# Performance work log

Measured on AMD Instinct MI355X. Metric: run time of the kernel, lower is better.

Reference implementation:

```python
import jax, jax.numpy as jnp
import numpy as np

VOCAB = 50257
EMBED = 128
B, S = 64, 4096


def setup_inputs() -> dict:
    key = jax.random.key(0)
    k1, k2, k3 = jax.random.split(key, 3)
    x = jax.random.randint(k1, (B, S), 0, VOCAB)
    # Linear(n_symboles, output_size) weight has shape [output_size, n_symboles]
    W = jax.random.normal(k2, (EMBED, VOCAB), dtype=jnp.float32) * 0.02
    b = jax.random.normal(k3, (EMBED,), dtype=jnp.float32) * 0.02
    return {"x": x, "W": W, "b": b}


def reference(x, W, b):
    # one_hot(x, V) @ W.T + b  ==  gather rows of W.T at x, then add bias.
    # Mathematically identical to the torch one-hot + Linear path, but
    # avoids materializing the [B, S, V] one-hot tensor.
    return W.T[x] + b  # [B, S, EMBED]
```

## Files before the change

### kernel.cpp

```cpp
#include <hip/hip_runtime.h>

#define VOCAB 50257
#define EMBED 128
#define NTOK  (64 * 4096)

typedef float    f32x4 __attribute__((ext_vector_type(4)));
typedef _Float16 f16x4 __attribute__((ext_vector_type(4)));
typedef _Float16 f16x8 __attribute__((ext_vector_type(8)));

__global__ void transpose_h_kernel(const float* __restrict__ W,
                                   const float* __restrict__ bias,
                                   _Float16* __restrict__ Wt) {
    __shared__ float tile[64][65];
    const int t  = threadIdx.x;
    const int v0 = blockIdx.x * 64;
    const int e0 = blockIdx.y * 64;
    const bool full = (v0 + 64 <= VOCAB);

    if (full) {
#pragma unroll
        for (int it = 0; it < 4; ++it) {
            const int e_loc = (t >> 4) + it * 16;
            const int c4    = (t & 15) * 4;
            f32x4 val = *(const f32x4*)&W[(size_t)(e0 + e_loc) * VOCAB + v0 + c4];
            tile[c4 + 0][e_loc] = val.x;
            tile[c4 + 1][e_loc] = val.y;
            tile[c4 + 2][e_loc] = val.z;
            tile[c4 + 3][e_loc] = val.w;
        }
    } else {
#pragma unroll
        for (int it = 0; it < 16; ++it) {
            const int e_loc = (t >> 6) + it * 4;
            const int c     = t & 63;
            const int v     = v0 + c;
            tile[c][e_loc] = (v < VOCAB) ? W[(size_t)(e0 + e_loc) * VOCAB + v]
                                         : 0.0f;
        }
    }
    __syncthreads();

    const int eo = (t & 7) * 8;
    const f32x4 ba = *(const f32x4*)&bias[e0 + eo];
    const f32x4 bb = *(const f32x4*)&bias[e0 + eo + 4];
#pragma unroll
    for (int it = 0; it < 2; ++it) {
        const int v_loc = (t >> 3) + it * 32;
        const int v     = v0 + v_loc;
        if (v < VOCAB) {
            f16x8 h;
            h[0] = (_Float16)(tile[v_loc][eo + 0] + ba.x);
            h[1] = (_Float16)(tile[v_loc][eo + 1] + ba.y);
            h[2] = (_Float16)(tile[v_loc][eo + 2] + ba.z);
            h[3] = (_Float16)(tile[v_loc][eo + 3] + ba.w);
            h[4] = (_Float16)(tile[v_loc][eo + 4] + bb.x);
            h[5] = (_Float16)(tile[v_loc][eo + 5] + bb.y);
            h[6] = (_Float16)(tile[v_loc][eo + 6] + bb.z);
            h[7] = (_Float16)(tile[v_loc][eo + 7] + bb.w);
            *(f16x8*)&Wt[(size_t)v * EMBED + e0 + eo] = h;
        }
    }
}

__global__ void gather_h_kernel(const int* __restrict__ x,
                                const f16x4* __restrict__ Wt,
                                f32x4* __restrict__ out) {
    const int gid    = blockIdx.x * blockDim.x + threadIdx.x;
    const int stride = gridDim.x * blockDim.x;

    int g[4], idx[4];
#pragma unroll
    for (int k = 0; k < 4; ++k) {
        g[k]   = gid + k * stride;
        idx[k] = x[g[k] >> 5];
    }
    f16x4 h[4];
#pragma unroll
    for (int k = 0; k < 4; ++k)
        h[k] = Wt[(size_t)idx[k] * 32 + (g[k] & 31)];
#pragma unroll
    for (int k = 0; k < 4; ++k) {
        f32x4 r;
        r.x = (float)h[k][0];
        r.y = (float)h[k][1];
        r.z = (float)h[k][2];
        r.w = (float)h[k][3];
        out[g[k]] = r;
    }
}

__global__ void direct_kernel(const int* __restrict__ x,
                              const float* __restrict__ W,
                              const float* __restrict__ bias,
                              f32x4* __restrict__ out) {
    const int gid   = blockIdx.x * blockDim.x + threadIdx.x;
    const int token = gid >> 5;
    const int e4    = gid & 31;
    const int idx   = x[token];
    const int e     = e4 * 4;
    f32x4 r;
    r.x = W[(size_t)(e + 0) * VOCAB + idx] + bias[e + 0];
    r.y = W[(size_t)(e + 1) * VOCAB + idx] + bias[e + 1];
    r.z = W[(size_t)(e + 2) * VOCAB + idx] + bias[e + 2];
    r.w = W[(size_t)(e + 3) * VOCAB + idx] + bias[e + 3];
    out[(size_t)token * 32 + e4] = r;
}

extern "C" void kernel_launch(void* const* d_in, const int* in_sizes, int n_in,
                              void* d_out, int out_size, void* d_ws, size_t ws_size,
                              hipStream_t stream) {
    const int*   x    = (const int*)d_in[0];
    const float* W    = (const float*)d_in[1];
    const float* bias = (const float*)d_in[2];

    const size_t wt_bytes = (size_t)VOCAB * EMBED * sizeof(_Float16);

    if (ws_size >= wt_bytes) {
        _Float16* Wt = (_Float16*)d_ws;
        dim3 tgrid((VOCAB + 63) / 64, 2);
        transpose_h_kernel<<<tgrid, 256, 0, stream>>>(W, bias, Wt);

        const int gblocks = (NTOK * 32 / 4) / 256;
        gather_h_kernel<<<gblocks, 256, 0, stream>>>(x, (const f16x4*)Wt,
                                                     (f32x4*)d_out);
    } else {
        const int dblocks = (NTOK * 32) / 256;
        direct_kernel<<<dblocks, 256, 0, stream>>>(x, W, bias, (f32x4*)d_out);
    }
}
```

Measured before the change: 46.94 us.

## Slice transposed fp16 table into embedding chunks for cache-local gather

The fp16 transposed weight table is now stored as 8 separate slices of 16 embedding columns each. The gather kernel assigns each block one slice for 64 tokens, so concurrently running blocks read a smaller working set (about 1.6 MB per slice) that fits in cache. The cost is narrower per-block work: each token's output row is now written in 64-byte pieces by different blocks, and the loop that processed several elements per thread is gone.

After: 45.72 us. 2.6% less time.

```diff
diff --git a/kernel.cpp b/kernel.cpp
--- a/kernel.cpp
+++ b/kernel.cpp
@@ -3,6 +3,7 @@
 #define VOCAB 50257
 #define EMBED 128
 #define NTOK  (64 * 4096)
+#define NSLICE 8
 
 typedef float    f32x4 __attribute__((ext_vector_type(4)));
 typedef _Float16 f16x4 __attribute__((ext_vector_type(4)));
@@ -41,8 +42,11 @@
     __syncthreads();
 
     const int eo = (t & 7) * 8;
-    const f32x4 ba = *(const f32x4*)&bias[e0 + eo];
-    const f32x4 bb = *(const f32x4*)&bias[e0 + eo + 4];
+    const int eg = e0 + eo;
+    const int s  = eg >> 4;
+    const int ep = eg & 15;
+    const f32x4 ba = *(const f32x4*)&bias[eg];
+    const f32x4 bb = *(const f32x4*)&bias[eg + 4];
 #pragma unroll
     for (int it = 0; it < 2; ++it) {
         const int v_loc = (t >> 3) + it * 32;
@@ -57,36 +61,28 @@
             h[5] = (_Float16)(tile[v_loc][eo + 5] + bb.y);
             h[6] = (_Float16)(tile[v_loc][eo + 6] + bb.z);
             h[7] = (_Float16)(tile[v_loc][eo + 7] + bb.w);
-            *(f16x8*)&Wt[(size_t)v * EMBED + e0 + eo] = h;
+            *(f16x8*)&Wt[((size_t)s * VOCAB + v) * 16 + ep] = h;
         }
     }
 }
 
-__global__ void gather_h_kernel(const int* __restrict__ x,
-                                const f16x4* __restrict__ Wt,
-                                f32x4* __restrict__ out) {
-    const int gid    = blockIdx.x * blockDim.x + threadIdx.x;
-    const int stride = gridDim.x * blockDim.x;
-
-    int g[4], idx[4];
-#pragma unroll
-    for (int k = 0; k < 4; ++k) {
-        g[k]   = gid + k * stride;
-        idx[k] = x[g[k] >> 5];
-    }
-    f16x4 h[4];
-#pragma unroll
-    for (int k = 0; k < 4; ++k)
-        h[k] = Wt[(size_t)idx[k] * 32 + (g[k] & 31)];
-#pragma unroll
-    for (int k = 0; k < 4; ++k) {
-        f32x4 r;
-        r.x = (float)h[k][0];
-        r.y = (float)h[k][1];
-        r.z = (float)h[k][2];
-        r.w = (float)h[k][3];
-        out[g[k]] = r;
-    }
+__global__ void gather_sliced_kernel(const int* __restrict__ x,
+                                     const f16x4* __restrict__ Wt,
+                                     f32x4* __restrict__ out) {
+    const int bid   = blockIdx.x;
+    const int slice = bid & (NSLICE - 1);
+    const int tblk  = bid >> 3;
+    const int t     = threadIdx.x;
+    const int tok   = tblk * 64 + (t >> 2);
+    const int q     = t & 3;
+    const int idx   = x[tok];
+    const f16x4 h = Wt[((size_t)slice * VOCAB + idx) * 4 + q];
+    f32x4 r;
+    r.x = (float)h[0];
+    r.y = (float)h[1];
+    r.z = (float)h[2];
+    r.w = (float)h[3];
+    out[(size_t)tok * 32 + slice * 4 + q] = r;
 }
 
 __global__ void direct_kernel(const int* __restrict__ x,
@@ -120,9 +116,9 @@
         dim3 tgrid((VOCAB + 63) / 64, 2);
         transpose_h_kernel<<<tgrid, 256, 0, stream>>>(W, bias, Wt);
 
-        const int gblocks = (NTOK * 32 / 4) / 256;
-        gather_h_kernel<<<gblocks, 256, 0, stream>>>(x, (const f16x4*)Wt,
-                                                     (f32x4*)d_out);
+        const int gblocks = (NTOK / 64) * NSLICE;
+        gather_sliced_kernel<<<gblocks, 256, 0, stream>>>(x, (const f16x4*)Wt,
+                                                          (f32x4*)d_out);
     } else {
         const int dblocks = (NTOK * 32) / 256;
         direct_kernel<<<dblocks, 256, 0, stream>>>(x, W, bias, (f32x4*)d_out);
```
